# Kernel optimization log

Hardware: AMD Instinct MI355X
Metric: run time of the kernel (lower is better)

The kernel has to match this reference:

```python
import jax, jax.numpy as jnp
import numpy as np

NQ, BS, NP_, D = 100, 8, 17, 256
NH, L, P = 8, 4, 4
DH = D // NH
DFF = 1024
SHAPES = [(92, 92), (46, 46), (23, 23), (12, 12)]
LEN_IN = sum(h * w for h, w in SHAPES)


def setup_inputs() -> dict:
    key = jax.random.key(0)
    ks = jax.random.split(key, 20)
    def nrm(k, shape, s=0.02):
        return jax.random.normal(k, shape, jnp.float32) * s
    return {
        "tgt_pose": jax.random.normal(ks[0], (NQ, BS, NP_, D), jnp.float32),
        "tgt_pose_query_pos": jax.random.normal(ks[1], (NQ, BS, NP_, D), jnp.float32),
        "tgt_pose_reference_points": jax.random.uniform(ks[2], (NQ, BS, NP_, L, 2), jnp.float32),
        "memory": jax.random.normal(ks[3], (BS, LEN_IN, D), jnp.float32),
        "w_in_w": nrm(ks[4], (3 * D, D)), "b_in_w": jnp.zeros((3 * D,), jnp.float32),
        "w_out_w": nrm(ks[5], (D, D)), "b_out_w": jnp.zeros((D,), jnp.float32),
        "w_in_a": nrm(ks[6], (3 * D, D)), "b_in_a": jnp.zeros((3 * D,), jnp.float32),
        "w_out_a": nrm(ks[7], (D, D)), "b_out_a": jnp.zeros((D,), jnp.float32),
        "w_off": nrm(ks[8], (NH * L * P * 2, D)), "b_off": nrm(ks[9], (NH * L * P * 2,), 0.1),
        "w_aw": nrm(ks[10], (NH * L * P, D)), "b_aw": jnp.zeros((NH * L * P,), jnp.float32),
        "w_val": nrm(ks[11], (D, D)), "b_val": jnp.zeros((D,), jnp.float32),
        "w_oc": nrm(ks[12], (D, D)), "b_oc": jnp.zeros((D,), jnp.float32),
        "g_w": jnp.ones((D,), jnp.float32), "be_w": jnp.zeros((D,), jnp.float32),
        "g_a": jnp.ones((D,), jnp.float32), "be_a": jnp.zeros((D,), jnp.float32),
        "g1": jnp.ones((D,), jnp.float32), "be1": jnp.zeros((D,), jnp.float32),
        "g2": jnp.ones((D,), jnp.float32), "be2": jnp.zeros((D,), jnp.float32),
        "w1": nrm(ks[13], (DFF, D)), "b1": jnp.zeros((DFF,), jnp.float32),
        "w2": nrm(ks[14], (D, DFF)), "b2": jnp.zeros((D,), jnp.float32),
        "memory_key_padding_mask": jnp.zeros((BS, LEN_IN), jnp.bool_),
        "memory_spatial_shapes": jnp.array(SHAPES, jnp.int32),
        "memory_level_start_index": jnp.array(np.cumsum([0] + [h * w for h, w in SHAPES[:-1]]), jnp.int32),
    }


def _ln(x, g, b, eps=1e-5):
    m = x.mean(-1, keepdims=True)
    v = ((x - m) ** 2).mean(-1, keepdims=True)
    return (x - m) * jax.lax.rsqrt(v + eps) * g + b


def _mha(q, k, v, w_in, b_in, w_out, b_out):
    # q,k,v: [B, S, D] batch-first; torch nn.MultiheadAttention math
    B, S, d = q.shape
    qp = (q @ w_in[:d].T + b_in[:d]).reshape(B, S, NH, DH)
    kp = (k @ w_in[d:2 * d].T + b_in[d:2 * d]).reshape(B, -1, NH, DH)
    vp = (v @ w_in[2 * d:].T + b_in[2 * d:]).reshape(B, -1, NH, DH)
    att = jax.nn.softmax(jnp.einsum('bqhd,bkhd->bhqk', qp, kp) / jnp.sqrt(jnp.float32(DH)), axis=-1)
    o = jnp.einsum('bhqk,bkhd->bqhd', att, vp).reshape(B, S, d)
    return o @ w_out.T + b_out


def _bilinear(v, loc, Hl, Wl):
    # v: [Hl*Wl, NH, DH]; loc: [Lq, NH, P, 2] normalized to [0,1]; grid_sample align_corners=False, zero pad
    x = loc[..., 0] * Wl - 0.5
    y = loc[..., 1] * Hl - 0.5
    x0 = jnp.floor(x); y0 = jnp.floor(y)
    wx = x - x0; wy = y - y0
    x0i = x0.astype(jnp.int32); y0i = y0.astype(jnp.int32)
    hid = jnp.arange(NH)[None, :, None]
    def tap(yi, xi, w):
        ok = (xi >= 0) & (xi < Wl) & (yi >= 0) & (yi < Hl)
        idx = jnp.clip(yi, 0, Hl - 1) * Wl + jnp.clip(xi, 0, Wl - 1)
        return jnp.where(ok[..., None], v[idx, hid], 0.0) * w[..., None]
    return (tap(y0i, x0i, (1 - wy) * (1 - wx)) + tap(y0i, x0i + 1, (1 - wy) * wx)
            + tap(y0i + 1, x0i, wy * (1 - wx)) + tap(y0i + 1, x0i + 1, wy * wx))


def _deform(query, ref, memory, mask, shapes, starts, w_off, b_off, w_aw, b_aw, w_val, b_val, w_oc, b_oc):
    # Multi-scale deformable attention (MSDeformAttn)
    bs, lq, d = query.shape
    value = memory @ w_val.T + b_val
    value = jnp.where(mask[..., None], 0.0, value).reshape(bs, -1, NH, DH)
    off = (query @ w_off.T + b_off).reshape(bs, lq, NH, L, P, 2)
    aw = jax.nn.softmax((query @ w_aw.T + b_aw).reshape(bs, lq, NH, L * P), axis=-1).reshape(bs, lq, NH, L, P)
    shp = np.asarray(shapes)
    st = np.asarray(starts)
    norm = jnp.asarray(shp[:, ::-1].copy(), jnp.float32)  # (W, H) per level
    loc = ref[:, :, None, :, None, :] + off / norm[None, None, None, :, None, :]
    out = jnp.zeros((bs, lq, NH, DH), query.dtype)
    for l in range(L):
        Hl, Wl = int(shp[l, 0]), int(shp[l, 1])
        v_l = value[:, int(st[l]):int(st[l]) + Hl * Wl]
        samp = jax.vmap(lambda vv, lo: _bilinear(vv, lo, Hl, Wl))(v_l, loc[:, :, :, l])
        out = out + jnp.einsum('bqhp,bqhpd->bqhd', aw[:, :, :, l], samp)
    return out.reshape(bs, lq, d) @ w_oc.T + b_oc


def _forward(tgt_pose, qpos, ref, memory, w_in_w, b_in_w, w_out_w, b_out_w, w_in_a, b_in_a, w_out_a, b_out_a, w_off, b_off, w_aw, b_aw, w_val, b_val, w_oc, b_oc, g_w, be_w, g_a, be_a, g1, be1, g2, be2, w1, b1, w2, b2, mask, shapes, starts):
    nq, bs, npt, d = tgt_pose.shape
    # within-group self-attn over keypoints (seq = np, batch = nq*bs)
    qk = (tgt_pose + qpos).reshape(nq * bs, npt, d)
    t2 = _mha(qk, qk, tgt_pose.reshape(nq * bs, npt, d), w_in_w, b_in_w, w_out_w, b_out_w).reshape(nq, bs, npt, d)
    x = _ln(tgt_pose + t2, g_w, be_w)
    # across-group self-attn over queries (seq = nq, batch = bs*np)
    y = x.reshape(nq, bs * npt, d).transpose(1, 0, 2)
    t2 = _mha(y, y, y, w_in_a, b_in_a, w_out_a, b_out_a).transpose(1, 0, 2).reshape(nq, bs, npt, d)
    x = _ln(x + t2, g_a, be_a)
    # multi-scale deformable cross-attn
    q = (x + qpos).transpose(1, 0, 2, 3).reshape(bs, nq * npt, d)
    r = ref.transpose(1, 0, 2, 3, 4).reshape(bs, nq * npt, L, 2)
    t2 = _deform(q, r, memory, mask, shapes, starts, w_off, b_off, w_aw, b_aw, w_val, b_val, w_oc, b_oc)
    t2 = t2.reshape(bs, nq, npt, d).transpose(1, 0, 2, 3)
    x = _ln(x + t2, g1, be1)
    # FFN
    ff = jax.nn.relu(x @ w1.T + b1) @ w2.T + b2
    return _ln(x + ff, g2, be2)


def reference(tgt_pose, tgt_pose_query_pos, tgt_pose_reference_points, memory, w_in_w, b_in_w, w_out_w, b_out_w, w_in_a, b_in_a, w_out_a, b_out_a, w_off, b_off, w_aw, b_aw, w_val, b_val, w_oc, b_oc, g_w, be_w, g_a, be_a, g1, be1, g2, be2, w1, b1, w2, b2, memory_key_padding_mask, memory_spatial_shapes, memory_level_start_index):
    return _forward(tgt_pose, tgt_pose_query_pos, tgt_pose_reference_points, memory, w_in_w, b_in_w, w_out_w, b_out_w, w_in_a, b_in_a, w_out_a, b_out_a, w_off, b_off, w_aw, b_aw, w_val, b_val, w_oc, b_oc, g_w, be_w, g_a, be_a, g1, be1, g2, be2, w1, b1, w2, b2, memory_key_padding_mask, memory_spatial_shapes, memory_level_start_index)
```

## Files before the change

### kernel.cpp

```cpp
#include <hip/hip_runtime.h>
#include <hip/hip_bf16.h>
#include <math.h>

#define NQd 100
#define BSd 8
#define NPTd 17
#define DIMd 256
#define NHd 8
#define DHd 32
#define DFFd 1024
#define NTOK (NQd*BSd*NPTd)
#define LENIN 11253
#define MTOK (BSd*LENIN)

typedef __attribute__((ext_vector_type(8))) short bf16x8;
typedef __attribute__((ext_vector_type(4))) short bf16x4s;
typedef __attribute__((ext_vector_type(4))) float f32x4;

__device__ inline short f2bs(float f) {
    __hip_bfloat16 h = __float2bfloat16(f);
    return *reinterpret_cast<short*>(&h);
}
__device__ inline float bs2f(short s) {
    return __uint_as_float(((unsigned)(unsigned short)s) << 16);
}

template<bool RELU, bool OUT_BF16, bool A_FP32>
__global__ __launch_bounds__(256)
void gemm_mfma(const void* __restrict__ Av, const __hip_bfloat16* __restrict__ W,
               const float* __restrict__ bias, void* __restrict__ Cv,
               int M, int N, int K, int ldc, int col0) {
    __shared__ __hip_bfloat16 LA[2][4][129][8];
    __shared__ __hip_bfloat16 LW[2][4][129][8];
    const int tid = threadIdx.x;
    const int lane = tid & 63, wave = tid >> 6;
    const int wr = wave >> 1, wc = wave & 1;
    const int m0 = blockIdx.y * 128, n0 = blockIdx.x * 128;
    const int l15 = lane & 15, lg = lane >> 4;
    const int srow = tid >> 2, koct = tid & 3;
    bf16x8 aReg[2], wReg[2];

    auto load_tile = [&](int k0) {
#pragma unroll
        for (int it = 0; it < 2; ++it) {
            const int row = srow + it * 64;
            const int gm = m0 + row;
            bf16x8 av = {0, 0, 0, 0, 0, 0, 0, 0};
            if (A_FP32) {
                if (gm < M) {
                    const float* ap = (const float*)Av + (size_t)gm * K + k0 + koct * 8;
                    float4 f0 = *(const float4*)ap;
                    float4 f1 = *(const float4*)(ap + 4);
                    av = (bf16x8){f2bs(f0.x), f2bs(f0.y), f2bs(f0.z), f2bs(f0.w),
                                  f2bs(f1.x), f2bs(f1.y), f2bs(f1.z), f2bs(f1.w)};
                }
            } else {
                if (gm < M)
                    av = *(const bf16x8*)((const __hip_bfloat16*)Av + (size_t)gm * K + k0 + koct * 8);
            }
            aReg[it] = av;
            wReg[it] = *(const bf16x8*)(W + (size_t)(n0 + row) * K + k0 + koct * 8);
        }
    };
    auto write_tile = [&](int buf) {
#pragma unroll
        for (int it = 0; it < 2; ++it) {
            const int row = srow + it * 64;
            *(bf16x8*)&LA[buf][koct][row][0] = aReg[it];
            *(bf16x8*)&LW[buf][koct][row][0] = wReg[it];
        }
    };

    f32x4 acc[4][4];
#pragma unroll
    for (int i = 0; i < 4; ++i)
#pragma unroll
        for (int j = 0; j < 4; ++j) acc[i][j] = (f32x4){0.f, 0.f, 0.f, 0.f};

    const int NT = K >> 5;
    load_tile(0);
    write_tile(0);
    __syncthreads();
    for (int t = 0; t < NT; ++t) {
        const int cur = t & 1;
        if (t + 1 < NT) load_tile((t + 1) * 32);
        bf16x8 af[4], bfr[4];
#pragma unroll
        for (int f = 0; f < 4; ++f) {
            af[f]  = *(const bf16x8*)&LA[cur][lg][wr * 64 + f * 16 + l15][0];
            bfr[f] = *(const bf16x8*)&LW[cur][lg][wc * 64 + f * 16 + l15][0];
        }
#pragma unroll
        for (int fm = 0; fm < 4; ++fm)
#pragma unroll
            for (int fn = 0; fn < 4; ++fn)
                acc[fm][fn] = __builtin_amdgcn_mfma_f32_16x16x32_bf16(af[fm], bfr[fn], acc[fm][fn], 0, 0, 0);
        if (t + 1 < NT) write_tile(cur ^ 1);
        __syncthreads();
    }

#pragma unroll
    for (int fm = 0; fm < 4; ++fm) {
        const int row = m0 + wr * 64 + fm * 16 + lg * 4;
#pragma unroll
        for (int fn = 0; fn < 4; ++fn) {
            const int coln = n0 + wc * 64 + fn * 16 + l15;
            const float bsv = bias[coln];
#pragma unroll
            for (int r = 0; r < 4; ++r) {
                const int gr = row + r;
                if (gr >= M) continue;
                float v = acc[fm][fn][r] + bsv;
                if (RELU) v = fmaxf(v, 0.f);
                if (OUT_BF16)
                    ((__hip_bfloat16*)Cv)[(size_t)gr * ldc + col0 + coln] = __float2bfloat16(v);
                else
                    ((float*)Cv)[(size_t)gr * ldc + col0 + coln] = v;
            }
        }
    }
}

template<bool A_FP32, bool OUT_BF16>
__global__ __launch_bounds__(256)
void gemm64(const void* __restrict__ Av, const __hip_bfloat16* __restrict__ W,
            const float* __restrict__ bias, void* __restrict__ Cv,
            int M, int K, int ldc, int col0) {
    __shared__ __hip_bfloat16 LA[2][4][65][8];
    __shared__ __hip_bfloat16 LW[2][4][65][8];
    const int tid = threadIdx.x;
    const int lane = tid & 63, wave = tid >> 6;
    const int wr = wave >> 1, wc = wave & 1;
    const int m0 = blockIdx.y * 64, n0 = blockIdx.x * 64;
    const int l15 = lane & 15, lg = lane >> 4;
    const int srow = tid >> 2, koct = tid & 3;
    const int gm = m0 + srow;
    const bool okA = gm < M;
    const __hip_bfloat16* pAb = (const __hip_bfloat16*)Av + (size_t)(okA ? gm : 0) * K + koct * 8;
    const float* pAf = (const float*)Av + (size_t)(okA ? gm : 0) * K + koct * 8;
    const __hip_bfloat16* pW = W + (size_t)(n0 + srow) * K + koct * 8;

    bf16x8 aR, wR;
    float4 f0R, f1R;
    auto load_tile = [&](int k0) {
        if (A_FP32) {
            f0R = okA ? *(const float4*)(pAf + k0)     : make_float4(0.f, 0.f, 0.f, 0.f);
            f1R = okA ? *(const float4*)(pAf + k0 + 4) : make_float4(0.f, 0.f, 0.f, 0.f);
        } else {
            aR = okA ? *(const bf16x8*)(pAb + k0) : (bf16x8){0, 0, 0, 0, 0, 0, 0, 0};
        }
        wR = *(const bf16x8*)(pW + k0);
    };
    auto write_tile = [&](int buf) {
        bf16x8 v;
        if (A_FP32)
            v = (bf16x8){f2bs(f0R.x), f2bs(f0R.y), f2bs(f0R.z), f2bs(f0R.w),
                         f2bs(f1R.x), f2bs(f1R.y), f2bs(f1R.z), f2bs(f1R.w)};
        else
            v = aR;
        *(bf16x8*)&LA[buf][koct][srow][0] = v;
        *(bf16x8*)&LW[buf][koct][srow][0] = wR;
    };

    f32x4 acc[2][2];
#pragma unroll
    for (int i = 0; i < 2; ++i)
#pragma unroll
        for (int j = 0; j < 2; ++j) acc[i][j] = (f32x4){0.f, 0.f, 0.f, 0.f};

    const int NT = K >> 5;
    load_tile(0);
    write_tile(0);
    __syncthreads();
    for (int t = 0; t < NT; ++t) {
        const int cur = t & 1;
        if (t + 1 < NT) load_tile((t + 1) * 32);
        bf16x8 af[2], bfr[2];
#pragma unroll
        for (int f = 0; f < 2; ++f) {
            af[f]  = *(const bf16x8*)&LA[cur][lg][wr * 32 + f * 16 + l15][0];
            bfr[f] = *(const bf16x8*)&LW[cur][lg][wc * 32 + f * 16 + l15][0];
        }
#pragma unroll
        for (int fm = 0; fm < 2; ++fm)
#pragma unroll
            for (int fn = 0; fn < 2; ++fn)
                acc[fm][fn] = __builtin_amdgcn_mfma_f32_16x16x32_bf16(af[fm], bfr[fn], acc[fm][fn], 0, 0, 0);
        if (t + 1 < NT) write_tile(cur ^ 1);
        __syncthreads();
    }

#pragma unroll
    for (int fm = 0; fm < 2; ++fm) {
        const int row = m0 + wr * 32 + fm * 16 + lg * 4;
#pragma unroll
        for (int fn = 0; fn < 2; ++fn) {
            const int coln = n0 + wc * 32 + fn * 16 + l15;
            const float bsv = bias[coln];
#pragma unroll
            for (int r = 0; r < 4; ++r) {
                const int gr = row + r;
                if (gr >= M) continue;
                float v = acc[fm][fn][r] + bsv;
                if (OUT_BF16)
                    ((__hip_bfloat16*)Cv)[(size_t)gr * ldc + col0 + coln] = __float2bfloat16(v);
                else
                    ((float*)Cv)[(size_t)gr * ldc + col0 + coln] = v;
            }
        }
    }
}

template<bool A_FP32, bool OUT_BF16>
__global__ __launch_bounds__(512)
void gemm64w(const void* __restrict__ Av, const __hip_bfloat16* __restrict__ W,
             const float* __restrict__ bias, void* __restrict__ Cv,
             int M, int K, int ldc, int col0) {
    __shared__ __hip_bfloat16 LA[2][4][65][8];
    const int tid = threadIdx.x;
    const int lane = tid & 63, wc = tid >> 6;
    const int m0 = blockIdx.x * 64;
    const int l15 = lane & 15, lg = lane >> 4;
    const int srow = (tid & 255) >> 2, koct = tid & 3;
    const bool stager = tid < 256;
    const int gm = m0 + srow;
    const bool okA = stager && (gm < M);
    const __hip_bfloat16* pAb = (const __hip_bfloat16*)Av + (size_t)(okA ? gm : 0) * K + koct * 8;
    const float* pAf = (const float*)Av + (size_t)(okA ? gm : 0) * K + koct * 8;
    const __hip_bfloat16* pW0 = W + (size_t)(wc * 32 + l15) * K + lg * 8;
    const __hip_bfloat16* pW1 = W + (size_t)(wc * 32 + 16 + l15) * K + lg * 8;

    bf16x8 aR;
    float4 f0R, f1R;
    auto load_tile = [&](int k0) {
        if (!stager) return;
        if (A_FP32) {
            f0R = okA ? *(const float4*)(pAf + k0)     : make_float4(0.f, 0.f, 0.f, 0.f);
            f1R = okA ? *(const float4*)(pAf + k0 + 4) : make_float4(0.f, 0.f, 0.f, 0.f);
        } else {
            aR = okA ? *(const bf16x8*)(pAb + k0) : (bf16x8){0, 0, 0, 0, 0, 0, 0, 0};
        }
    };
    auto write_tile = [&](int buf) {
        if (!stager) return;
        bf16x8 v;
        if (A_FP32)
            v = (bf16x8){f2bs(f0R.x), f2bs(f0R.y), f2bs(f0R.z), f2bs(f0R.w),
                         f2bs(f1R.x), f2bs(f1R.y), f2bs(f1R.z), f2bs(f1R.w)};
        else
            v = aR;
        *(bf16x8*)&LA[buf][koct][srow][0] = v;
    };

    f32x4 acc[4][2];
#pragma unroll
    for (int i = 0; i < 4; ++i) {
        acc[i][0] = (f32x4){0.f, 0.f, 0.f, 0.f};
        acc[i][1] = (f32x4){0.f, 0.f, 0.f, 0.f};
    }

    const int NT = K >> 5;
    load_tile(0);
    write_tile(0);
    __syncthreads();
    for (int t = 0; t < NT; ++t) {
        const int cur = t & 1;
        if (t + 1 < NT) load_tile((t + 1) * 32);
        bf16x8 b0 = *(const bf16x8*)(pW0 + t * 32);
        bf16x8 b1 = *(const bf16x8*)(pW1 + t * 32);
        bf16x8 af[4];
#pragma unroll
        for (int fm = 0; fm < 4; ++fm)
            af[fm] = *(const bf16x8*)&LA[cur][lg][fm * 16 + l15][0];
#pragma unroll
        for (int fm = 0; fm < 4; ++fm) {
            acc[fm][0] = __builtin_amdgcn_mfma_f32_16x16x32_bf16(af[fm], b0, acc[fm][0], 0, 0, 0);
            acc[fm][1] = __builtin_amdgcn_mfma_f32_16x16x32_bf16(af[fm], b1, acc[fm][1], 0, 0, 0);
        }
        if (t + 1 < NT) write_tile(cur ^ 1);
        __syncthreads();
    }

#pragma unroll
    for (int fm = 0; fm < 4; ++fm) {
        const int row = m0 + fm * 16 + lg * 4;
#pragma unroll
        for (int fn = 0; fn < 2; ++fn) {
            const int coln = wc * 32 + fn * 16 + l15;
            const float bsv = bias[coln];
#pragma unroll
            for (int r = 0; r < 4; ++r) {
                const int gr = row + r;
                if (gr >= M) continue;
                float v = acc[fm][fn][r] + bsv;
                if (OUT_BF16)
                    ((__hip_bfloat16*)Cv)[(size_t)gr * ldc + col0 + coln] = __float2bfloat16(v);
                else
                    ((float*)Cv)[(size_t)gr * ldc + col0 + coln] = v;
            }
        }
    }
}

__global__ void cvt_weights(const float* w0, const float* w1, const float* w2,
                            const float* w3, const float* w4, const float* w5,
                            const float* w6, const float* w7, const float* w8,
                            const float* w9, __hip_bfloat16* dst) {
    int idx = blockIdx.x * 256 + threadIdx.x;
    float v;
    if      (idx <  196608) v = w0[idx];
    else if (idx <  262144) v = w1[idx -  196608];
    else if (idx <  458752) v = w2[idx -  262144];
    else if (idx <  524288) v = w3[idx -  458752];
    else if (idx <  589824) v = w4[idx -  524288];
    else if (idx <  622592) v = w5[idx -  589824];
    else if (idx <  688128) v = w6[idx -  622592];
    else if (idx <  753664) v = w7[idx -  688128];
    else if (idx < 1015808) v = w8[idx -  753664];
    else                    v = w9[idx - 1015808];
    dst[idx] = __float2bfloat16(v);
}

__global__ void gather_rows_b(const float* __restrict__ src, const float* __restrict__ add,
                              __hip_bfloat16* __restrict__ dst, int mode) {
    int t = blockIdx.x, c = threadIdx.x;
    int r;
    if (mode == 0) r = t;
    else if (mode == 1) { int m = t / 100, q = t % 100; r = q * 136 + m; }
    else { int b = t / 1700, jj = t % 1700; int q = jj / 17, p = jj % 17; r = q * 136 + b * 17 + p; }
    float v = src[(size_t)r * 256 + c];
    if (add) v += add[(size_t)r * 256 + c];
    dst[(size_t)t * 256 + c] = __float2bfloat16(v);
}

__global__ void attn17(const float* __restrict__ qkv, __hip_bfloat16* __restrict__ out) {
    const int g = blockIdx.x, h = blockIdx.y;
    __shared__ float q[17][32], k[17][32], v[17][32], s[17][18];
    const int tid = threadIdx.x;
    for (int idx = tid; idx < 17 * 32; idx += 256) {
        int i = idx >> 5, d = idx & 31;
        size_t row = (size_t)(g * 17 + i) * 768 + h * 32 + d;
        q[i][d] = qkv[row];
        k[i][d] = qkv[row + 256];
        v[i][d] = qkv[row + 512];
    }
    __syncthreads();
    for (int idx = tid; idx < 17 * 17; idx += 256) {
        int i = idx / 17, j = idx % 17;
        float acc = 0.f;
#pragma unroll
        for (int d = 0; d < 32; ++d) acc += q[i][d] * k[j][d];
        s[i][j] = acc * 0.17677669529663688f;
    }
    __syncthreads();
    if (tid < 17) {
        float m = -1e30f;
        for (int j = 0; j < 17; ++j) m = fmaxf(m, s[tid][j]);
        float sum = 0.f;
        for (int j = 0; j < 17; ++j) { float e = __expf(s[tid][j] - m); s[tid][j] = e; sum += e; }
        float inv = 1.f / sum;
        for (int j = 0; j < 17; ++j) s[tid][j] *= inv;
    }
    __syncthreads();
    for (int idx = tid; idx < 17 * 32; idx += 256) {
        int i = idx >> 5, d = idx & 31;
        float acc = 0.f;
        for (int j = 0; j < 17; ++j) acc += s[i][j] * v[j][d];
        out[(size_t)(g * 17 + i) * 256 + h * 32 + d] = __float2bfloat16(acc);
    }
}

__global__ __launch_bounds__(128)
void attn100(const float* __restrict__ qkv, __hip_bfloat16* __restrict__ out) {
    const int g = blockIdx.x, h = blockIdx.y;
    __shared__ float Ks[100][32], Vs[100][32];
    const int tid = threadIdx.x;
    for (int idx = tid; idx < 800; idx += 128) {
        int j = idx >> 3, qd = (idx & 7) * 4;
        const float* base = qkv + (size_t)(g * 100 + j) * 768 + h * 32;
        *(float4*)&Ks[j][qd] = *(const float4*)(base + 256 + qd);
        *(float4*)&Vs[j][qd] = *(const float4*)(base + 512 + qd);
    }
    __syncthreads();
    if (tid >= 100) return;
    const float* qp = qkv + (size_t)(g * 100 + tid) * 768 + h * 32;
    float q[32];
#pragma unroll
    for (int d4 = 0; d4 < 32; d4 += 4) {
        float4 v = *(const float4*)(qp + d4);
        q[d4] = v.x; q[d4 + 1] = v.y; q[d4 + 2] = v.z; q[d4 + 3] = v.w;
    }
    float m = -1e30f, l = 0.f, o[32];
#pragma unroll
    for (int d = 0; d < 32; ++d) o[d] = 0.f;
    for (int j = 0; j < 100; ++j) {
        float s = 0.f;
#pragma unroll
        for (int d = 0; d < 32; ++d) s += q[d] * Ks[j][d];
        s *= 0.17677669529663688f;
        float nm = fmaxf(m, s);
        float f = __expf(m - nm), p = __expf(s - nm);
        l = l * f + p;
#pragma unroll
        for (int d = 0; d < 32; ++d) o[d] = o[d] * f + p * Vs[j][d];
        m = nm;
    }
    float inv = 1.f / l;
    __hip_bfloat16* op = out + (size_t)(g * 100 + tid) * 256 + h * 32;
#pragma unroll
    for (int d = 0; d < 32; ++d) op[d] = __float2bfloat16(o[d] * inv);
}

#define TPB 4
__global__ __launch_bounds__(256)
void deform_sample(const __hip_bfloat16* __restrict__ value, const float* __restrict__ off,
                   const float* __restrict__ aw, const float* __restrict__ ref,
                   __hip_bfloat16* __restrict__ out) {
    const int t0 = blockIdx.x * TPB;
    const int tid = threadIdx.x;
    __shared__ float raw[TPB][128];
    __shared__ float wgt[TPB][128];
    __shared__ int   cidx[TPB][128][4];
    __shared__ float cw[TPB][128][4];

    for (int idx = tid; idx < TPB * 128; idx += 256) {
        int tk = idx >> 7, i = idx & 127;
        raw[tk][i] = aw[(size_t)(t0 + tk) * 128 + i];
    }
    __syncthreads();
    if (tid < TPB * 8) {
        int tk = tid >> 3, h = tid & 7;
        float m = -1e30f;
        for (int i = 0; i < 16; ++i) m = fmaxf(m, raw[tk][h * 16 + i]);
        float sum = 0.f;
        float e[16];
        for (int i = 0; i < 16; ++i) { e[i] = __expf(raw[tk][h * 16 + i] - m); sum += e[i]; }
        float inv = 1.f / sum;
        for (int i = 0; i < 16; ++i) wgt[tk][h * 16 + i] = e[i] * inv;
    }
    __syncthreads();

    const int Hs[4] = {92, 46, 23, 12};
    const int Sts[4] = {0, 8464, 10580, 11109};
    for (int s = tid; s < TPB * 128; s += 256) {
        int tk = s >> 7, sid = s & 127;
        int t = t0 + tk;
        int b = t / 1700, jj = t % 1700;
        int q = jj / 17, p = jj % 17;
        int l = (sid >> 2) & 3;
        int HW = Hs[l];
        float HWf = (float)HW;
        const float* refp = ref + (size_t)((q * 8 + b) * 17 + p) * 8;
        float rx = refp[l * 2], ry = refp[l * 2 + 1];
        float ox = off[(size_t)t * 256 + sid * 2];
        float oy = off[(size_t)t * 256 + sid * 2 + 1];
        float x = (rx + ox / HWf) * HWf - 0.5f;
        float y = (ry + oy / HWf) * HWf - 0.5f;
        float x0f = floorf(x), y0f = floorf(y);
        float wx = x - x0f, wy = y - y0f;
        int xi = (int)x0f, yi = (int)y0f;
        float wg = wgt[tk][sid];
#pragma unroll
        for (int c = 0; c < 4; ++c) {
            int cy = c >> 1, cx = c & 1;
            int yy = yi + cy, xx = xi + cx;
            bool ok = (xx >= 0) && (xx < HW) && (yy >= 0) && (yy < HW);
            int yc = min(max(yy, 0), HW - 1);
            int xc = min(max(xx, 0), HW - 1);
            cidx[tk][sid][c] = Sts[l] + yc * HW + xc;
            float w = (cy ? wy : 1.f - wy) * (cx ? wx : 1.f - wx);
            cw[tk][sid][c] = ok ? wg * w : 0.f;
        }
    }
    __syncthreads();

    const int tk = tid >> 6, lane = tid & 63;
    const int h = lane >> 3, d4 = (lane & 7) * 4;
    const int t = t0 + tk;
    const int b = t / 1700;
    const __hip_bfloat16* vb = value + (size_t)b * LENIN * 256 + h * 32 + d4;
    float4 acc = make_float4(0.f, 0.f, 0.f, 0.f);
    for (int s16 = 0; s16 < 16; ++s16) {
        int sid = h * 16 + s16;
#pragma unroll
        for (int c = 0; c < 4; ++c) {
            int idx = cidx[tk][sid][c];
            float w = cw[tk][sid][c];
            bf16x4s v = *(const bf16x4s*)(vb + (size_t)idx * 256);
            acc.x += w * bs2f(v.x); acc.y += w * bs2f(v.y);
            acc.z += w * bs2f(v.z); acc.w += w * bs2f(v.w);
        }
    }
    __hip_bfloat16* op = out + (size_t)t * 256 + h * 32 + d4;
    op[0] = __float2bfloat16(acc.x);
    op[1] = __float2bfloat16(acc.y);
    op[2] = __float2bfloat16(acc.z);
    op[3] = __float2bfloat16(acc.w);
}

__global__ __launch_bounds__(256)
void res_ln(const float* __restrict__ res, const float* __restrict__ proj,
            const float* __restrict__ g, const float* __restrict__ be,
            float* __restrict__ out, __hip_bfloat16* __restrict__ outb, int mode) {
    const int wave = threadIdx.x >> 6, lane = threadIdx.x & 63;
    const int r = blockIdx.x * 4 + wave;
    int t;
    if (mode == 0) t = r;
    else if (mode == 1) { int q = r / 136, m = r % 136; t = m * 100 + q; }
    else { int q = r / 136, rem = r % 136; int b = rem / 17, p = rem % 17; t = b * 1700 + q * 17 + p; }
    const int c4 = lane * 4;
    float4 a = *(const float4*)&res[(size_t)r * 256 + c4];
    float4 p = *(const float4*)&proj[(size_t)t * 256 + c4];
    float v[4] = {a.x + p.x, a.y + p.y, a.z + p.z, a.w + p.w};
    float s = v[0] + v[1] + v[2] + v[3];
#pragma unroll
    for (int off = 32; off > 0; off >>= 1) s += __shfl_xor(s, off);
    float mean = s * (1.f / 256.f);
    float d[4], ss = 0.f;
#pragma unroll
    for (int i = 0; i < 4; ++i) { d[i] = v[i] - mean; ss += d[i] * d[i]; }
#pragma unroll
    for (int off = 32; off > 0; off >>= 1) ss += __shfl_xor(ss, off);
    float rs = rsqrtf(ss * (1.f / 256.f) + 1e-5f);
    float4 gv = *(const float4*)&g[c4];
    float4 bv = *(const float4*)&be[c4];
    float o0 = d[0] * rs * gv.x + bv.x;
    float o1 = d[1] * rs * gv.y + bv.y;
    float o2 = d[2] * rs * gv.z + bv.z;
    float o3 = d[3] * rs * gv.w + bv.w;
    *(float4*)&out[(size_t)r * 256 + c4] = make_float4(o0, o1, o2, o3);
    if (outb) {
        bf16x4s ob = {f2bs(o0), f2bs(o1), f2bs(o2), f2bs(o3)};
        *(bf16x4s*)&outb[(size_t)r * 256 + c4] = ob;
    }
}

extern "C" void kernel_launch(void* const* d_in, const int* in_sizes, int n_in,
                              void* d_out, int out_size, void* d_ws, size_t ws_size,
                              hipStream_t stream) {
    const float* tgt    = (const float*)d_in[0];
    const float* qpos   = (const float*)d_in[1];
    const float* ref    = (const float*)d_in[2];
    const float* memory = (const float*)d_in[3];
    const float* w_in_w = (const float*)d_in[4];
    const float* b_in_w = (const float*)d_in[5];
    const float* w_out_w= (const float*)d_in[6];
    const float* b_out_w= (const float*)d_in[7];
    const float* w_in_a = (const float*)d_in[8];
    const float* b_in_a = (const float*)d_in[9];
    const float* w_out_a= (const float*)d_in[10];
    const float* b_out_a= (const float*)d_in[11];
    const float* w_off  = (const float*)d_in[12];
    const float* b_off  = (const float*)d_in[13];
    const float* w_aw   = (const float*)d_in[14];
    const float* b_aw   = (const float*)d_in[15];
    const float* w_val  = (const float*)d_in[16];
    const float* b_val  = (const float*)d_in[17];
    const float* w_oc   = (const float*)d_in[18];
    const float* b_oc   = (const float*)d_in[19];
    const float* g_w    = (const float*)d_in[20];
    const float* be_w   = (const float*)d_in[21];
    const float* g_a    = (const float*)d_in[22];
    const float* be_a   = (const float*)d_in[23];
    const float* g1     = (const float*)d_in[24];
    const float* be1    = (const float*)d_in[25];
    const float* g2     = (const float*)d_in[26];
    const float* be2    = (const float*)d_in[27];
    const float* w1     = (const float*)d_in[28];
    const float* b1     = (const float*)d_in[29];
    const float* w2     = (const float*)d_in[30];
    const float* b2     = (const float*)d_in[31];

    float* X  = (float*)d_out;
    float* ws = (float*)d_ws;
    float* R1 = ws;
    float* R2 = R1 + (size_t)MTOK * 256;
    float* R3 = R2 + (size_t)NTOK * 256;
    float* R6 = R3 + (size_t)NTOK * 128;
    float* QBF= R6 + (size_t)NTOK * 128;
    float* WBF= QBF+ (size_t)NTOK * 128;

    __hip_bfloat16* R3b = (__hip_bfloat16*)R3;
    __hip_bfloat16* Qb  = (__hip_bfloat16*)QBF;
    __hip_bfloat16* Wb  = (__hip_bfloat16*)WBF;
    __hip_bfloat16* Hb  = (__hip_bfloat16*)R1;
    __hip_bfloat16* Vb  = (__hip_bfloat16*)R1;

    __hip_bfloat16* w_in_w_b  = Wb;
    __hip_bfloat16* w_out_w_b = Wb +  196608;
    __hip_bfloat16* w_in_a_b  = Wb +  262144;
    __hip_bfloat16* w_out_a_b = Wb +  458752;
    __hip_bfloat16* w_off_b   = Wb +  524288;
    __hip_bfloat16* w_aw_b    = Wb +  589824;
    __hip_bfloat16* w_val_b   = Wb +  622592;
    __hip_bfloat16* w_oc_b    = Wb +  688128;
    __hip_bfloat16* w1_b      = Wb +  753664;
    __hip_bfloat16* w2_b      = Wb + 1015808;

    cvt_weights<<<4992, 256, 0, stream>>>(w_in_w, w_out_w, w_in_a, w_out_a, w_off,
                                          w_aw, w_val, w_oc, w1, w2, Wb);

    const int MY64 = (NTOK + 63) / 64;

    gather_rows_b<<<NTOK, 256, 0, stream>>>(tgt, qpos, Qb, 0);
    gemm_mfma<false, false, false><<<dim3(4, (NTOK + 127) / 128), 256, 0, stream>>>(
        Qb, w_in_w_b, b_in_w, R1, NTOK, 512, 256, 768, 0);
    gemm64<true, false><<<dim3(4, MY64), 256, 0, stream>>>(
        tgt, w_in_w_b + 512 * 256, b_in_w + 512, R1, NTOK, 256, 768, 512);
    attn17<<<dim3(800, 8), 256, 0, stream>>>(R1, R3b);
    gemm64<false, false><<<dim3(4, MY64), 256, 0, stream>>>(
        R3b, w_out_w_b, b_out_w, R2, NTOK, 256, 256, 0);
    res_ln<<<NTOK / 4, 256, 0, stream>>>(tgt, R2, g_w, be_w, X, nullptr, 0);

    gather_rows_b<<<NTOK, 256, 0, stream>>>(X, nullptr, Qb, 1);
    gemm_mfma<false, false, false><<<dim3(6, (NTOK + 127) / 128), 256, 0, stream>>>(
        Qb, w_in_a_b, b_in_a, R1, NTOK, 768, 256, 768, 0);
    attn100<<<dim3(136, 8), 128, 0, stream>>>(R1, R3b);
    gemm64<false, false><<<dim3(4, MY64), 256, 0, stream>>>(
        R3b, w_out_a_b, b_out_a, R2, NTOK, 256, 256, 0);
    res_ln<<<NTOK / 4, 256, 0, stream>>>(X, R2, g_a, be_a, X, nullptr, 1);

    gemm64w<true, true><<<(MTOK + 63) / 64, 512, 0, stream>>>(
        memory, w_val_b, b_val, Vb, MTOK, 256, 256, 0);
    gather_rows_b<<<NTOK, 256, 0, stream>>>(X, qpos, Qb, 2);
    gemm64<false, false><<<dim3(4, MY64), 256, 0, stream>>>(
        Qb, w_off_b, b_off, R2, NTOK, 256, 256, 0);
    gemm64<false, false><<<dim3(2, MY64), 256, 0, stream>>>(
        Qb, w_aw_b, b_aw, R6, NTOK, 256, 128, 0);
    deform_sample<<<NTOK / TPB, 256, 0, stream>>>(Vb, R2, R6, ref, R3b);
    gemm64<false, false><<<dim3(4, MY64), 256, 0, stream>>>(
        R3b, w_oc_b, b_oc, R2, NTOK, 256, 256, 0);
    res_ln<<<NTOK / 4, 256, 0, stream>>>(X, R2, g1, be1, X, Qb, 2);

    gemm_mfma<true, true, false><<<dim3(8, (NTOK + 127) / 128), 256, 0, stream>>>(
        Qb, w1_b, b1, Hb, NTOK, 1024, 256, 1024, 0);
    gemm64<false, false><<<dim3(4, MY64), 256, 0, stream>>>(
        (const __hip_bfloat16*)Hb, w2_b, b2, R2, NTOK, 1024, 256, 0);
    res_ln<<<NTOK / 4, 256, 0, stream>>>(X, R2, g2, be2, X, nullptr, 0);
}
```

Baseline: 372.6 us.

## Rewrite 100-token self-attention kernel with bf16 MFMA for QK^T and PV

Replaces the per-thread scalar online-softmax attention over 100 keys with a wave-level version. Q·K^T and P·V are computed with 16x16x32 bf16 MFMA instructions, and the softmax row reductions use lane shuffles. V is stored transposed in shared memory as bf16 and the probabilities are staged per wave, with padding to 112/128 columns. This removes most of the scalar FMA work, at the cost of bf16 rounding of Q, K, V and P, and it leaves three of the seven row tiles on one wave and four on the other.

```diff
diff --git a/kernel.cpp b/kernel.cpp
--- a/kernel.cpp
+++ b/kernel.cpp
@@ -23,6 +23,12 @@
 }
 __device__ inline float bs2f(short s) {
     return __uint_as_float(((unsigned)(unsigned short)s) << 16);
+}
+__device__ inline bf16x8 cvt8(const float* p) {
+    float4 f0 = *(const float4*)p;
+    float4 f1 = *(const float4*)(p + 4);
+    return (bf16x8){f2bs(f0.x), f2bs(f0.y), f2bs(f0.z), f2bs(f0.w),
+                    f2bs(f1.x), f2bs(f1.y), f2bs(f1.z), f2bs(f1.w)};
 }
 
 template<bool RELU, bool OUT_BF16, bool A_FP32>
@@ -373,42 +379,98 @@
 __global__ __launch_bounds__(128)
 void attn100(const float* __restrict__ qkv, __hip_bfloat16* __restrict__ out) {
     const int g = blockIdx.x, h = blockIdx.y;
-    __shared__ float Ks[100][32], Vs[100][32];
+    __shared__ __hip_bfloat16 Vt[32][136];
+    __shared__ __hip_bfloat16 Pl[2][16][136];
     const int tid = threadIdx.x;
-    for (int idx = tid; idx < 800; idx += 128) {
-        int j = idx >> 3, qd = (idx & 7) * 4;
-        const float* base = qkv + (size_t)(g * 100 + j) * 768 + h * 32;
-        *(float4*)&Ks[j][qd] = *(const float4*)(base + 256 + qd);
-        *(float4*)&Vs[j][qd] = *(const float4*)(base + 512 + qd);
-    }
-    __syncthreads();
-    if (tid >= 100) return;
-    const float* qp = qkv + (size_t)(g * 100 + tid) * 768 + h * 32;
-    float q[32];
-#pragma unroll
-    for (int d4 = 0; d4 < 32; d4 += 4) {
-        float4 v = *(const float4*)(qp + d4);
-        q[d4] = v.x; q[d4 + 1] = v.y; q[d4 + 2] = v.z; q[d4 + 3] = v.w;
-    }
-    float m = -1e30f, l = 0.f, o[32];
-#pragma unroll
-    for (int d = 0; d < 32; ++d) o[d] = 0.f;
-    for (int j = 0; j < 100; ++j) {
-        float s = 0.f;
-#pragma unroll
-        for (int d = 0; d < 32; ++d) s += q[d] * Ks[j][d];
-        s *= 0.17677669529663688f;
-        float nm = fmaxf(m, s);
-        float f = __expf(m - nm), p = __expf(s - nm);
-        l = l * f + p;
-#pragma unroll
-        for (int d = 0; d < 32; ++d) o[d] = o[d] * f + p * Vs[j][d];
-        m = nm;
-    }
-    float inv = 1.f / l;
-    __hip_bfloat16* op = out + (size_t)(g * 100 + tid) * 256 + h * 32;
-#pragma unroll
-    for (int d = 0; d < 32; ++d) op[d] = __float2bfloat16(o[d] * inv);
+    const int wave = tid >> 6, lane = tid & 63;
+    const int l15 = lane & 15, lg = lane >> 4;
+
+    for (int idx = tid; idx < 3200; idx += 128) {
+        int j = idx >> 5, d = idx & 31;
+        Vt[d][j] = __float2bfloat16(qkv[(size_t)(g * 100 + j) * 768 + 512 + h * 32 + d]);
+    }
+    for (int idx = tid; idx < 32 * 28; idx += 128) {
+        int d = idx & 31, jz = 100 + (idx >> 5);
+        Vt[d][jz] = __float2bfloat16(0.f);
+    }
+    __syncthreads();
+
+    const int rt0 = wave ? 4 : 0, rt1 = wave ? 7 : 4;
+    for (int rt = rt0; rt < rt1; ++rt) {
+        const int rowbase = rt * 16;
+        int qr = rowbase + l15; if (qr > 99) qr = 99;
+        bf16x8 aq = cvt8(qkv + (size_t)(g * 100 + qr) * 768 + h * 32 + lg * 8);
+        f32x4 s[7];
+#pragma unroll
+        for (int jt = 0; jt < 7; ++jt) {
+            int jr = jt * 16 + l15; if (jr > 99) jr = 99;
+            bf16x8 bk = cvt8(qkv + (size_t)(g * 100 + jr) * 768 + 256 + h * 32 + lg * 8);
+            s[jt] = __builtin_amdgcn_mfma_f32_16x16x32_bf16(aq, bk, (f32x4){0.f, 0.f, 0.f, 0.f}, 0, 0, 0);
+        }
+        float mr[4] = {-1e30f, -1e30f, -1e30f, -1e30f};
+#pragma unroll
+        for (int jt = 0; jt < 7; ++jt) {
+            const bool valid = (jt * 16 + l15) < 100;
+#pragma unroll
+            for (int r = 0; r < 4; ++r) {
+                float v = valid ? s[jt][r] * 0.17677669529663688f : -1e30f;
+                s[jt][r] = v;
+                mr[r] = fmaxf(mr[r], v);
+            }
+        }
+#pragma unroll
+        for (int r = 0; r < 4; ++r) {
+            mr[r] = fmaxf(mr[r], __shfl_xor(mr[r], 1));
+            mr[r] = fmaxf(mr[r], __shfl_xor(mr[r], 2));
+            mr[r] = fmaxf(mr[r], __shfl_xor(mr[r], 4));
+            mr[r] = fmaxf(mr[r], __shfl_xor(mr[r], 8));
+        }
+        float lr[4] = {0.f, 0.f, 0.f, 0.f};
+#pragma unroll
+        for (int jt = 0; jt < 7; ++jt)
+#pragma unroll
+            for (int r = 0; r < 4; ++r) {
+                float e = __expf(s[jt][r] - mr[r]);
+                s[jt][r] = e;
+                lr[r] += e;
+            }
+#pragma unroll
+        for (int r = 0; r < 4; ++r) {
+            lr[r] += __shfl_xor(lr[r], 1);
+            lr[r] += __shfl_xor(lr[r], 2);
+            lr[r] += __shfl_xor(lr[r], 4);
+            lr[r] += __shfl_xor(lr[r], 8);
+        }
+#pragma unroll
+        for (int jt = 0; jt < 7; ++jt)
+#pragma unroll
+            for (int r = 0; r < 4; ++r)
+                Pl[wave][lg * 4 + r][jt * 16 + l15] = __float2bfloat16(s[jt][r]);
+#pragma unroll
+        for (int r = 0; r < 4; ++r)
+            Pl[wave][lg * 4 + r][112 + l15] = __float2bfloat16(0.f);
+
+        f32x4 o0 = (f32x4){0.f, 0.f, 0.f, 0.f};
+        f32x4 o1 = (f32x4){0.f, 0.f, 0.f, 0.f};
+#pragma unroll
+        for (int c = 0; c < 4; ++c) {
+            bf16x8 pa = *(const bf16x8*)&Pl[wave][l15][c * 32 + lg * 8];
+            bf16x8 v0 = *(const bf16x8*)&Vt[l15][c * 32 + lg * 8];
+            bf16x8 v1 = *(const bf16x8*)&Vt[16 + l15][c * 32 + lg * 8];
+            o0 = __builtin_amdgcn_mfma_f32_16x16x32_bf16(pa, v0, o0, 0, 0, 0);
+            o1 = __builtin_amdgcn_mfma_f32_16x16x32_bf16(pa, v1, o1, 0, 0, 0);
+        }
+#pragma unroll
+        for (int r = 0; r < 4; ++r) {
+            int row = rowbase + lg * 4 + r;
+            if (row < 100) {
+                float inv = 1.f / lr[r];
+                __hip_bfloat16* op = out + (size_t)(g * 100 + row) * 256 + h * 32;
+                op[l15]      = __float2bfloat16(o0[r] * inv);
+                op[16 + l15] = __float2bfloat16(o1[r] * inv);
+            }
+        }
+    }
 }
 
 #define TPB 4
```

Measured after the change: 333.8 us. 10.4% less time.
